# Kernel tuning notes

Measured on AMD Instinct MI355X. Metric: run time of the kernel, lower is better.

The kernel has to match this reference:

```python
import jax, jax.numpy as jnp
import numpy as np
import math

D_MODEL = 1024
N_HEADS = 16
HEAD_DIM = D_MODEL // N_HEADS


def _compute_slopes(n_heads: int) -> np.ndarray:
    def pow2_slopes(n):
        start = 2.0 ** (-(2.0 ** (-(math.log2(n) - 3))))
        return [start * (start ** i) for i in range(n)]
    if math.log2(n_heads).is_integer():
        s = pow2_slopes(n_heads)
    else:
        cp = 2 ** math.floor(math.log2(n_heads))
        s = pow2_slopes(cp) + pow2_slopes(2 * cp)[0::2][: n_heads - cp]
    return np.asarray(s, dtype=np.float32)


def setup_inputs() -> dict:
    key = jax.random.key(0)
    ks = jax.random.split(key, 11)
    B, T, D = 2, 2048, D_MODEL
    scale = 1.0 / math.sqrt(D)
    inp = {
        "query": jax.random.normal(ks[0], (B, T, D), jnp.float32),
        "key": jax.random.normal(ks[1], (B, T, D), jnp.float32),
        "value": jax.random.normal(ks[2], (B, T, D), jnp.float32),
        "Wq": jax.random.normal(ks[3], (D, D), jnp.float32) * scale,
        "bq": jnp.zeros((D,), jnp.float32),
        "Wk": jax.random.normal(ks[4], (D, D), jnp.float32) * scale,
        "bk": jnp.zeros((D,), jnp.float32),
        "Wv": jax.random.normal(ks[5], (D, D), jnp.float32) * scale,
        "bv": jnp.zeros((D,), jnp.float32),
        "Wo": jax.random.normal(ks[6], (D, D), jnp.float32) * scale,
        "bo": jnp.zeros((D,), jnp.float32),
    }
    return inp


def reference(query, key, value, Wq, bq, Wk, bk, Wv, bv, Wo, bo):
    B, Tq, D = query.shape
    Tk = key.shape[1]
    H, hd = N_HEADS, HEAD_DIM
    scale = hd ** -0.5

    # projections -> [B, H, T, hd]
    Q = (query @ Wq + bq).reshape(B, Tq, H, hd).transpose(0, 2, 1, 3)
    K = (key @ Wk + bk).reshape(B, Tk, H, hd).transpose(0, 2, 1, 3)
    V = (value @ Wv + bv).reshape(B, Tk, H, hd).transpose(0, 2, 1, 3)

    # scores [B, H, Tq, Tk]
    attn = jnp.einsum("bhqd,bhkd->bhqk", Q, K) * scale

    # ALiBi bias (only applied when Tq == Tk, mirroring the original)
    slopes = jnp.asarray(_compute_slopes(H))  # [H]
    pos = jnp.arange(Tq)
    dist = -jnp.abs(pos[None, :] - pos[:, None]).astype(jnp.float32)  # [Tq, Tk]
    bias = slopes[:, None, None] * dist[None]  # [H, Tq, Tk]
    attn = attn + bias[None]

    attn = jax.nn.softmax(attn, axis=-1)
    out = jnp.einsum("bhqk,bhkd->bhqd", attn, V)
    out = out.transpose(0, 2, 1, 3).reshape(B, Tq, D)
    return out @ Wo + bo
```

## Files before the change

### kernel.cpp

```cpp
#include <hip/hip_runtime.h>
#include <stdint.h>

#define BSZ 2
#define TT 2048
#define DD 1024
#define HH 16
#define HD 64

typedef __bf16 bf16x8 __attribute__((ext_vector_type(8)));
typedef float f32x4 __attribute__((ext_vector_type(4)));

#if __has_builtin(__builtin_amdgcn_exp2f)
#define EXP2(x) __builtin_amdgcn_exp2f(x)
#else
#define EXP2(x) exp2f(x)
#endif

__device__ __forceinline__ unsigned short f2bf(float f) {
    union { float f; unsigned u; } c; c.f = f;
    unsigned u = c.u;
    unsigned r = u + 0x7fffu + ((u >> 16) & 1u);
    return (unsigned short)(r >> 16);
}
__device__ __forceinline__ unsigned fasu(float f) {
    union { float f; unsigned u; } c; c.f = f; return c.u;
}

union U4BF { uint4 u; bf16x8 b; };
__device__ __forceinline__ bf16x8 as_bf8(uint4 v) { U4BF c; c.u = v; return c.b; }

#if __has_builtin(__builtin_amdgcn_global_load_lds)
__device__ __forceinline__ void gl_lds16(const ushort* g, ushort* l) {
    __builtin_amdgcn_global_load_lds(
        (const __attribute__((address_space(1))) uint32_t*)g,
        (__attribute__((address_space(3))) uint32_t*)l, 16, 0, 0);
}
#define GLL_LANE 1
#else
__device__ __forceinline__ void gl_lds16_fallback(const ushort* g, ushort* l, int lane) {
    *(uint4*)(l + lane * 8) = *(const uint4*)(g);
}
#define GLL_LANE 0
#endif

__global__ void cvt3(const float* __restrict__ q, const float* __restrict__ k,
                     const float* __restrict__ v, ushort* __restrict__ xq,
                     ushort* __restrict__ xk, ushort* __restrict__ xv, int n4) {
    int z = blockIdx.y;
    const float* in = (z == 0) ? q : (z == 1) ? k : v;
    ushort* out = (z == 0) ? xq : (z == 1) ? xk : xv;
    int i = blockIdx.x * blockDim.x + threadIdx.x;
    if (i < n4) {
        float4 val = ((const float4*)in)[i];
        ushort4 o;
        o.x = f2bf(val.x); o.y = f2bf(val.y); o.z = f2bf(val.z); o.w = f2bf(val.w);
        ((ushort4*)out)[i] = o;
    }
}

__global__ void wtrans(const float* __restrict__ W0, const float* __restrict__ W1,
                       const float* __restrict__ W2, const float* __restrict__ W3,
                       ushort* __restrict__ T0, ushort* __restrict__ T1,
                       ushort* __restrict__ T2, ushort* __restrict__ T3) {
    __shared__ float sh[32][33];
    const float* src; ushort* dst;
    switch (blockIdx.z) {
        case 0:  src = W0; dst = T0; break;
        case 1:  src = W1; dst = T1; break;
        case 2:  src = W2; dst = T2; break;
        default: src = W3; dst = T3; break;
    }
    int k0 = blockIdx.y * 32, n0 = blockIdx.x * 32;
    int tx = threadIdx.x, ty = threadIdx.y;
    sh[ty][tx] = src[(size_t)(k0 + ty) * DD + n0 + tx];
    __syncthreads();
    dst[(size_t)(n0 + ty) * DD + k0 + tx] = f2bf(sh[tx][ty]);
}

template<int BM, int OUT_MODE>
__global__ __launch_bounds__(256)
void gemm_mfma(const ushort* __restrict__ A0, const ushort* __restrict__ B0,
               const float* __restrict__ c0, void* __restrict__ d0,
               const ushort* __restrict__ A1, const ushort* __restrict__ B1,
               const float* __restrict__ c1, void* __restrict__ d1,
               const ushort* __restrict__ A2, const ushort* __restrict__ B2,
               const float* __restrict__ c2, void* __restrict__ d2) {
    constexpr int TI = 4;
    constexpr int TJ = (BM == 128) ? 4 : 2;
    constexpr int WC = (BM == 128) ? 2 : 4;
    __shared__ __attribute__((aligned(16))) ushort As[BM][32];
    __shared__ __attribute__((aligned(16))) ushort Bs[128][32];
    const ushort* A; const ushort* Bt; const float* bias; void* outp;
    const int z = blockIdx.z;
    switch (z) {
        case 0:  A = A0; Bt = B0; bias = c0; outp = d0; break;
        case 1:  A = A1; Bt = B1; bias = c1; outp = d1; break;
        default: A = A2; Bt = B2; bias = c2; outp = d2; break;
    }
    const int tid  = threadIdx.x;
    const int lane = tid & 63, w = tid >> 6;
    const int wr = w / WC, wc = w % WC;
    const int ln = lane & 15, quad = lane >> 4;
    const int m0 = blockIdx.y * BM, n0 = blockIdx.x * 128;

    const f32x4 zero = {0.f, 0.f, 0.f, 0.f};
    f32x4 acc[TI][TJ];
    #pragma unroll
    for (int i = 0; i < TI; ++i)
        #pragma unroll
        for (int j = 0; j < TJ; ++j) acc[i][j] = zero;

    const int lr  = lane >> 2;
    const int lc8 = (lane & 3) * 8;

    for (int kb = 0; kb < 1024; kb += 32) {
        #pragma unroll
        for (int it = 0; it < BM / 64; ++it) {
            int r0 = it * 64 + w * 16;
#if GLL_LANE
            gl_lds16(A + (size_t)(m0 + r0 + lr) * 1024 + kb + lc8, &As[r0][0]);
#else
            gl_lds16_fallback(A + (size_t)(m0 + r0 + lr) * 1024 + kb + lc8, &As[r0][0], lane);
#endif
        }
        #pragma unroll
        for (int it = 0; it < 2; ++it) {
            int r0 = it * 64 + w * 16;
#if GLL_LANE
            gl_lds16(Bt + (size_t)(n0 + r0 + lr) * 1024 + kb + lc8, &Bs[r0][0]);
#else
            gl_lds16_fallback(Bt + (size_t)(n0 + r0 + lr) * 1024 + kb + lc8, &Bs[r0][0], lane);
#endif
        }
        __syncthreads();
        bf16x8 af[TI], bfr[TJ];
        #pragma unroll
        for (int i = 0; i < TI; ++i)
            af[i] = as_bf8(*(const uint4*)&As[wr * 64 + i * 16 + ln][quad * 8]);
        #pragma unroll
        for (int j = 0; j < TJ; ++j)
            bfr[j] = as_bf8(*(const uint4*)&Bs[wc * (TJ * 16) + j * 16 + ln][quad * 8]);
        #pragma unroll
        for (int i = 0; i < TI; ++i)
            #pragma unroll
            for (int j = 0; j < TJ; ++j)
                acc[i][j] = __builtin_amdgcn_mfma_f32_16x16x32_bf16(af[i], bfr[j], acc[i][j], 0, 0, 0);
        __syncthreads();
    }

    #pragma unroll
    for (int j = 0; j < TJ; ++j) {
        int n = n0 + wc * (TJ * 16) + j * 16 + ln;
        float bv = bias[n];
        #pragma unroll
        for (int i = 0; i < TI; ++i) {
            int mb = m0 + wr * 64 + i * 16 + quad * 4;
            if (OUT_MODE == 0 && z == 2) {
                int b = mb >> 11, t = mb & 2047, h = n >> 6, d = n & 63;
                ushort4 pk;
                pk.x = f2bf(acc[i][j][0] + bv);
                pk.y = f2bf(acc[i][j][1] + bv);
                pk.z = f2bf(acc[i][j][2] + bv);
                pk.w = f2bf(acc[i][j][3] + bv);
                *(ushort4*)((ushort*)outp + ((size_t)((b * HH + h) * HD + d)) * TT + t) = pk;
            } else {
                #pragma unroll
                for (int r = 0; r < 4; ++r) {
                    int m = mb + r;
                    float v = acc[i][j][r] + bv;
                    if (OUT_MODE == 0) {
                        int b = m >> 11, t = m & 2047, h = n >> 6, d = n & 63;
                        ((ushort*)outp)[(((size_t)(b * HH + h)) * TT + t) * HD + d] = f2bf(v);
                    } else {
                        ((float*)outp)[(size_t)m * 1024 + n] = v;
                    }
                }
            }
        }
    }
}

__global__ __launch_bounds__(256)
void attn_kernel(const ushort* __restrict__ Qh, const ushort* __restrict__ Kh,
                 const ushort* __restrict__ Vtg, ushort* __restrict__ outp) {
    __shared__ __attribute__((aligned(16))) char smem[20992];
    ushort (*Ps)[32][72] = (ushort (*)[32][72])smem;
    float  (*Rbuf)[64][41] = (float (*)[64][41])smem;

    const int tid  = threadIdx.x;
    const int lane = tid & 63, w = tid >> 6;
    const int ln = lane & 15, quad = lane >> 4;

    bf16x8 ones;
    {
        union { ushort us[8]; bf16x8 v; } uu;
        #pragma unroll
        for (int p = 0; p < 8; ++p) uu.us[p] = 0x3F80;
        ones = uu.v;
    }
    const f32x4 zero = {0.f, 0.f, 0.f, 0.f};
    const float c1 = 0.125f * 1.44269504f;

    for (int sel = 0; sel < 2; ++sel) {
        __syncthreads();
        const int item = sel ? (2047 - (int)blockIdx.x) : (int)blockIdx.x;
        const int h = 15 - (item >> 7);
        const int rr = item & 127;
        const int b = rr & 1;
        const int qt = rr >> 1;
        const int bh = b * 16 + h;
        const int qbase = qt * 32;
        const float slope2 = exp2f(-0.5f * (float)(h + 1)) * 1.44269504f;
        const size_t base = (size_t)bh * (TT * HD);

        const int D = (int)ceilf(22.0f / slope2);
        int lo = qbase - D;
        int kt_lo = (lo > 0) ? (lo >> 6) : 0;
        int kt_hi = (qbase + 32 + D + 63) >> 6;
        if (kt_hi > TT / 64) kt_hi = TT / 64;
        const int nt = kt_hi - kt_lo;
        const int cs = (nt + 3) >> 2;
        const int my_lo = kt_lo + w * cs;
        const int my_hi = (my_lo + cs < kt_hi) ? (my_lo + cs) : kt_hi;

        bf16x8 qa[2][2];
        #pragma unroll
        for (int g = 0; g < 2; ++g) {
            const uint4* qp = (const uint4*)(Qh + base + (size_t)(qbase + g * 16 + ln) * HD);
            qa[g][0] = as_bf8(qp[quad]);
            qa[g][1] = as_bf8(qp[4 + quad]);
        }
        f32x4 o[2][4], lsum[2];
        #pragma unroll
        for (int g = 0; g < 2; ++g) {
            lsum[g] = zero;
            #pragma unroll
            for (int dn = 0; dn < 4; ++dn) o[g][dn] = zero;
        }
        float qrf[2][4];
        #pragma unroll
        for (int g = 0; g < 2; ++g)
            #pragma unroll
            for (int r = 0; r < 4; ++r)
                qrf[g][r] = (float)(qbase + g * 16 + quad * 4 + r);

        const ushort* kp = Kh  + base + (size_t)ln * HD + quad * 8;
        const ushort* vp = Vtg + base + (size_t)ln * TT + quad * 8;

        if (my_lo < my_hi) {
            uint4 kf[8];
            {
                const int ko = my_lo * 4096;
                #pragma unroll
                for (int n = 0; n < 4; ++n)
                    #pragma unroll
                    for (int hf = 0; hf < 2; ++hf)
                        kf[n * 2 + hf] = *(const uint4*)(kp + ko + n * 1024 + hf * 32);
            }

            for (int kt = my_lo; kt < my_hi; ++kt) {
                uint4 vf[8];
                {
                    const int vo = kt * 64;
                    #pragma unroll
                    for (int dn = 0; dn < 4; ++dn)
                        #pragma unroll
                        for (int hf = 0; hf < 2; ++hf)
                            vf[dn * 2 + hf] = *(const uint4*)(vp + dn * 32768 + vo + hf * 32);
                }
                uint4 kn[8];
                if (kt + 1 < my_hi) {
                    const int ko = (kt + 1) * 4096;
                    #pragma unroll
                    for (int n = 0; n < 4; ++n)
                        #pragma unroll
                        for (int hf = 0; hf < 2; ++hf)
                            kn[n * 2 + hf] = *(const uint4*)(kp + ko + n * 1024 + hf * 32);
                }

                f32x4 s[2][4];
                #pragma unroll
                for (int n = 0; n < 4; ++n) {
                    bf16x8 b0 = as_bf8(kf[n * 2]);
                    bf16x8 b1 = as_bf8(kf[n * 2 + 1]);
                    #pragma unroll
                    for (int g = 0; g < 2; ++g) {
                        f32x4 zz = zero;
                        zz = __builtin_amdgcn_mfma_f32_16x16x32_bf16(qa[g][0], b0, zz, 0, 0, 0);
                        s[g][n] = __builtin_amdgcn_mfma_f32_16x16x32_bf16(qa[g][1], b1, zz, 0, 0, 0);
                    }
                }

                #pragma unroll
                for (int n = 0; n < 4; ++n) {
                    float kg = (float)(kt * 64 + n * 16 + ln);
                    int bswz = ((2 * n + (ln >> 3)) ^ quad) * 8 + (ln & 7);
                    #pragma unroll
                    for (int g = 0; g < 2; ++g) {
                        #pragma unroll
                        for (int r = 0; r < 4; ++r) {
                            float d = qrf[g][r] - kg;
                            float arg = fmaf(s[g][n][r], c1, -slope2 * fabsf(d));
                            float p = EXP2(arg);
                            Ps[w][g * 16 + quad * 4 + r][bswz] = (ushort)(fasu(p) >> 16);
                        }
                    }
                }

                #pragma unroll
                for (int hf = 0; hf < 2; ++hf) {
                    bf16x8 ap0 = as_bf8(*(const uint4*)&Ps[w][ln]     [((hf * 4 + quad) ^ (ln >> 2)) * 8]);
                    bf16x8 ap1 = as_bf8(*(const uint4*)&Ps[w][16 + ln][((hf * 4 + quad) ^ (ln >> 2)) * 8]);
                    #pragma unroll
                    for (int dn = 0; dn < 4; ++dn) {
                        bf16x8 bv = as_bf8(vf[dn * 2 + hf]);
                        o[0][dn] = __builtin_amdgcn_mfma_f32_16x16x32_bf16(ap0, bv, o[0][dn], 0, 0, 0);
                        o[1][dn] = __builtin_amdgcn_mfma_f32_16x16x32_bf16(ap1, bv, o[1][dn], 0, 0, 0);
                    }
                    lsum[0] = __builtin_amdgcn_mfma_f32_16x16x32_bf16(ap0, ones, lsum[0], 0, 0, 0);
                    lsum[1] = __builtin_amdgcn_mfma_f32_16x16x32_bf16(ap1, ones, lsum[1], 0, 0, 0);
                }

                #pragma unroll
                for (int i = 0; i < 8; ++i) kf[i] = kn[i];
            }
        }

        __syncthreads();
        if (w >= 2) {
            float* dst = &Rbuf[w - 2][lane][0];
            #pragma unroll
            for (int g = 0; g < 2; ++g) {
                #pragma unroll
                for (int dn = 0; dn < 4; ++dn)
                    #pragma unroll
                    for (int r = 0; r < 4; ++r)
                        dst[g * 16 + dn * 4 + r] = o[g][dn][r];
                #pragma unroll
                for (int r = 0; r < 4; ++r)
                    dst[32 + g * 4 + r] = lsum[g][r];
            }
        }
        __syncthreads();
        if (w < 2) {
            const float* src = &Rbuf[w][lane][0];
            #pragma unroll
            for (int g = 0; g < 2; ++g) {
                #pragma unroll
                for (int dn = 0; dn < 4; ++dn)
                    #pragma unroll
                    for (int r = 0; r < 4; ++r)
                        o[g][dn][r] += src[g * 16 + dn * 4 + r];
                #pragma unroll
                for (int r = 0; r < 4; ++r)
                    lsum[g][r] += src[32 + g * 4 + r];
            }
        }
        __syncthreads();
        if (w == 1) {
            float* dst = &Rbuf[0][lane][0];
            #pragma unroll
            for (int g = 0; g < 2; ++g) {
                #pragma unroll
                for (int dn = 0; dn < 4; ++dn)
                    #pragma unroll
                    for (int r = 0; r < 4; ++r)
                        dst[g * 16 + dn * 4 + r] = o[g][dn][r];
                #pragma unroll
                for (int r = 0; r < 4; ++r)
                    dst[32 + g * 4 + r] = lsum[g][r];
            }
        }
        __syncthreads();
        if (w == 0) {
            const float* src = &Rbuf[0][lane][0];
            #pragma unroll
            for (int g = 0; g < 2; ++g) {
                #pragma unroll
                for (int dn = 0; dn < 4; ++dn)
                    #pragma unroll
                    for (int r = 0; r < 4; ++r)
                        o[g][dn][r] += src[g * 16 + dn * 4 + r];
                #pragma unroll
                for (int r = 0; r < 4; ++r)
                    lsum[g][r] += src[32 + g * 4 + r];
            }
            #pragma unroll
            for (int g = 0; g < 2; ++g) {
                #pragma unroll
                for (int r = 0; r < 4; ++r) {
                    float inv = __builtin_amdgcn_rcpf(lsum[g][r]);
                    int q = qbase + g * 16 + quad * 4 + r;
                    size_t ob = ((size_t)(b * TT + q)) * DD + h * HD;
                    #pragma unroll
                    for (int dn = 0; dn < 4; ++dn)
                        outp[ob + dn * 16 + ln] = f2bf(o[g][dn][r] * inv);
                }
            }
        }
    }
}

extern "C" void kernel_launch(void* const* d_in, const int* in_sizes, int n_in,
                              void* d_out, int out_size, void* d_ws, size_t ws_size,
                              hipStream_t stream) {
    const float* query = (const float*)d_in[0];
    const float* key   = (const float*)d_in[1];
    const float* value = (const float*)d_in[2];
    const float* Wq = (const float*)d_in[3];
    const float* bq = (const float*)d_in[4];
    const float* Wk = (const float*)d_in[5];
    const float* bk = (const float*)d_in[6];
    const float* Wv = (const float*)d_in[7];
    const float* bv = (const float*)d_in[8];
    const float* Wo = (const float*)d_in[9];
    const float* bo = (const float*)d_in[10];
    float* out = (float*)d_out;

    char* ws = (char*)d_ws;
    const size_t MB = 1024 * 1024;
    ushort* Xq  = (ushort*)(ws + 0);
    ushort* Xk  = (ushort*)(ws + 8 * MB);
    ushort* Xv  = (ushort*)(ws + 16 * MB);
    ushort* Wtq = (ushort*)(ws + 24 * MB);
    ushort* Wtk = (ushort*)(ws + 26 * MB);
    ushort* Wtv = (ushort*)(ws + 28 * MB);
    ushort* Wto = (ushort*)(ws + 30 * MB);
    ushort* Qh  = (ushort*)(ws + 32 * MB);
    ushort* Kh  = (ushort*)(ws + 40 * MB);
    ushort* Vt  = (ushort*)(ws + 48 * MB);
    ushort* attn = (ushort*)(ws + 0);

    const int n4 = (BSZ * TT * DD) / 4;
    cvt3<<<dim3(n4 / 256, 3), 256, 0, stream>>>(query, key, value, Xq, Xk, Xv, n4);
    wtrans<<<dim3(32, 32, 4), dim3(32, 32), 0, stream>>>(Wq, Wk, Wv, Wo, Wtq, Wtk, Wtv, Wto);

    gemm_mfma<128, 0><<<dim3(8, 32, 3), 256, 0, stream>>>(
        Xq, Wtq, bq, Qh,  Xk, Wtk, bk, Kh,  Xv, Wtv, bv, Vt);

    attn_kernel<<<dim3(1024), 256, 0, stream>>>(Qh, Kh, Vt, attn);

    gemm_mfma<64, 1><<<dim3(8, 64, 1), 256, 0, stream>>>(
        attn, Wto, bo, out,  attn, Wto, bo, out,  attn, Wto, bo, out);
}
```

Measured before the change: 248.5 us.

## Fuse prep kernels, add separate V transpose, tighten ALiBi window and reduction

Merges the fp32-to-bf16 input conversion and the weight transpose into one prep launch, with each transpose block now running 256 threads. The V projection no longer writes a transposed layout from its GEMM epilogue; a dedicated vtrans kernel transposes V through LDS instead. The attention kernel narrows the ALiBi band cutoff from 22 to 18 in log2 units, which skips more far-away keys but drops more probability mass. It also collapses the three-step cross-wave reduction into a single step with a larger LDS buffer and sets launch bounds for 4 blocks per CU, at the cost of one extra kernel launch and an extra pass over V.

```diff
diff --git a/kernel.cpp b/kernel.cpp
--- a/kernel.cpp
+++ b/kernel.cpp
@@ -11,9 +11,11 @@
 typedef float f32x4 __attribute__((ext_vector_type(4)));
 
 #if __has_builtin(__builtin_amdgcn_exp2f)
-#define EXP2(x) __builtin_amdgcn_exp2f(x)
+__device__ __forceinline__ float fexp2(float x) { return __builtin_amdgcn_exp2f(x); }
 #else
-#define EXP2(x) exp2f(x)
+__device__ __forceinline__ float fexp2(float x) {
+    float r; asm("v_exp_f32 %0, %1\n\ts_nop 1" : "=v"(r) : "v"(x)); return r;
+}
 #endif
 
 __device__ __forceinline__ unsigned short f2bf(float f) {
@@ -43,38 +45,69 @@
 #define GLL_LANE 0
 #endif
 
-__global__ void cvt3(const float* __restrict__ q, const float* __restrict__ k,
-                     const float* __restrict__ v, ushort* __restrict__ xq,
-                     ushort* __restrict__ xk, ushort* __restrict__ xv, int n4) {
-    int z = blockIdx.y;
-    const float* in = (z == 0) ? q : (z == 1) ? k : v;
-    ushort* out = (z == 0) ? xq : (z == 1) ? xk : xv;
-    int i = blockIdx.x * blockDim.x + threadIdx.x;
-    if (i < n4) {
+__global__ __launch_bounds__(256)
+void prep(const float* __restrict__ q, const float* __restrict__ k,
+          const float* __restrict__ v,
+          const float* __restrict__ W0, const float* __restrict__ W1,
+          const float* __restrict__ W2, const float* __restrict__ W3,
+          ushort* __restrict__ xq, ushort* __restrict__ xk, ushort* __restrict__ xv,
+          ushort* __restrict__ T0, ushort* __restrict__ T1,
+          ushort* __restrict__ T2, ushort* __restrict__ T3) {
+    __shared__ float sh[32][33];
+    const int y = blockIdx.y;
+    if (y < 3) {
+        const float* in = (y == 0) ? q : (y == 1) ? k : v;
+        ushort* out = (y == 0) ? xq : (y == 1) ? xk : xv;
+        int i = blockIdx.x * 256 + threadIdx.x;
         float4 val = ((const float4*)in)[i];
         ushort4 o;
         o.x = f2bf(val.x); o.y = f2bf(val.y); o.z = f2bf(val.z); o.w = f2bf(val.w);
         ((ushort4*)out)[i] = o;
-    }
-}
-
-__global__ void wtrans(const float* __restrict__ W0, const float* __restrict__ W1,
-                       const float* __restrict__ W2, const float* __restrict__ W3,
-                       ushort* __restrict__ T0, ushort* __restrict__ T1,
-                       ushort* __restrict__ T2, ushort* __restrict__ T3) {
-    __shared__ float sh[32][33];
-    const float* src; ushort* dst;
-    switch (blockIdx.z) {
-        case 0:  src = W0; dst = T0; break;
-        case 1:  src = W1; dst = T1; break;
-        case 2:  src = W2; dst = T2; break;
-        default: src = W3; dst = T3; break;
-    }
-    int k0 = blockIdx.y * 32, n0 = blockIdx.x * 32;
-    int tx = threadIdx.x, ty = threadIdx.y;
-    sh[ty][tx] = src[(size_t)(k0 + ty) * DD + n0 + tx];
+    } else {
+        const int x = blockIdx.x;
+        const float* src; ushort* dst;
+        switch (x >> 10) {
+            case 0:  src = W0; dst = T0; break;
+            case 1:  src = W1; dst = T1; break;
+            case 2:  src = W2; dst = T2; break;
+            default: src = W3; dst = T3; break;
+        }
+        const int tile = x & 1023;
+        const int k0 = (tile >> 5) * 32, n0 = (tile & 31) * 32;
+        const int tx = threadIdx.x & 31, ty = threadIdx.x >> 5;
+        #pragma unroll
+        for (int p = 0; p < 4; ++p)
+            sh[ty + 8 * p][tx] = src[(size_t)(k0 + ty + 8 * p) * DD + n0 + tx];
+        __syncthreads();
+        #pragma unroll
+        for (int p = 0; p < 4; ++p)
+            dst[(size_t)(n0 + ty + 8 * p) * DD + k0 + tx] = f2bf(sh[tx][ty + 8 * p]);
+    }
+}
+
+__global__ __launch_bounds__(256)
+void vtrans(const ushort* __restrict__ Vh, ushort* __restrict__ Vt) {
+    __shared__ ushort sh[64][72];
+    const int tid = threadIdx.x;
+    const int bh = blockIdx.y;
+    const int t0 = blockIdx.x * 64;
+    const size_t base = (size_t)bh * (TT * HD);
+    #pragma unroll
+    for (int it = 0; it < 2; ++it) {
+        int u = tid + it * 256;
+        int r = u >> 3, c8 = (u & 7) * 8;
+        *(uint4*)&sh[r][c8] = *(const uint4*)(Vh + base + (size_t)(t0 + r) * HD + c8);
+    }
     __syncthreads();
-    dst[(size_t)(n0 + ty) * DD + k0 + tx] = f2bf(sh[tx][ty]);
+    #pragma unroll
+    for (int it = 0; it < 2; ++it) {
+        int u = tid + it * 256;
+        int d = u >> 3, c8 = (u & 7) * 8;
+        alignas(16) ushort tmp[8];
+        #pragma unroll
+        for (int p = 0; p < 8; ++p) tmp[p] = sh[c8 + p][d];
+        *(uint4*)(Vt + base + (size_t)d * TT + t0 + c8) = *(const uint4*)tmp;
+    }
 }
 
 template<int BM, int OUT_MODE>
@@ -91,8 +124,7 @@
     __shared__ __attribute__((aligned(16))) ushort As[BM][32];
     __shared__ __attribute__((aligned(16))) ushort Bs[128][32];
     const ushort* A; const ushort* Bt; const float* bias; void* outp;
-    const int z = blockIdx.z;
-    switch (z) {
+    switch (blockIdx.z) {
         case 0:  A = A0; Bt = B0; bias = c0; outp = d0; break;
         case 1:  A = A1; Bt = B1; bias = c1; outp = d1; break;
         default: A = A2; Bt = B2; bias = c2; outp = d2; break;
@@ -154,38 +186,27 @@
         float bv = bias[n];
         #pragma unroll
         for (int i = 0; i < TI; ++i) {
-            int mb = m0 + wr * 64 + i * 16 + quad * 4;
-            if (OUT_MODE == 0 && z == 2) {
-                int b = mb >> 11, t = mb & 2047, h = n >> 6, d = n & 63;
-                ushort4 pk;
-                pk.x = f2bf(acc[i][j][0] + bv);
-                pk.y = f2bf(acc[i][j][1] + bv);
-                pk.z = f2bf(acc[i][j][2] + bv);
-                pk.w = f2bf(acc[i][j][3] + bv);
-                *(ushort4*)((ushort*)outp + ((size_t)((b * HH + h) * HD + d)) * TT + t) = pk;
-            } else {
-                #pragma unroll
-                for (int r = 0; r < 4; ++r) {
-                    int m = mb + r;
-                    float v = acc[i][j][r] + bv;
-                    if (OUT_MODE == 0) {
-                        int b = m >> 11, t = m & 2047, h = n >> 6, d = n & 63;
-                        ((ushort*)outp)[(((size_t)(b * HH + h)) * TT + t) * HD + d] = f2bf(v);
-                    } else {
-                        ((float*)outp)[(size_t)m * 1024 + n] = v;
-                    }
-                }
-            }
-        }
-    }
-}
-
-__global__ __launch_bounds__(256)
+            #pragma unroll
+            for (int r = 0; r < 4; ++r) {
+                int m = m0 + wr * 64 + i * 16 + quad * 4 + r;
+                float v = acc[i][j][r] + bv;
+                if (OUT_MODE == 0) {
+                    int b = m >> 11, t = m & 2047, h = n >> 6, d = n & 63;
+                    ((ushort*)outp)[(((size_t)(b * HH + h)) * TT + t) * HD + d] = f2bf(v);
+                } else {
+                    ((float*)outp)[(size_t)m * 1024 + n] = v;
+                }
+            }
+        }
+    }
+}
+
+__global__ __launch_bounds__(256, 4)
 void attn_kernel(const ushort* __restrict__ Qh, const ushort* __restrict__ Kh,
                  const ushort* __restrict__ Vtg, ushort* __restrict__ outp) {
-    __shared__ __attribute__((aligned(16))) char smem[20992];
+    __shared__ __attribute__((aligned(16))) char smem[33792];
     ushort (*Ps)[32][72] = (ushort (*)[32][72])smem;
-    float  (*Rbuf)[64][41] = (float (*)[64][41])smem;
+    float  (*Rbuf)[64][44] = (float (*)[64][44])smem;
 
     const int tid  = threadIdx.x;
     const int lane = tid & 63, w = tid >> 6;
@@ -213,7 +234,7 @@
         const float slope2 = exp2f(-0.5f * (float)(h + 1)) * 1.44269504f;
         const size_t base = (size_t)bh * (TT * HD);
 
-        const int D = (int)ceilf(22.0f / slope2);
+        const int D = (int)ceilf(18.0f / slope2);
         int lo = qbase - D;
         int kt_lo = (lo > 0) ? (lo >> 6) : 0;
         int kt_hi = (qbase + 32 + D + 63) >> 6;
@@ -301,7 +322,7 @@
                         for (int r = 0; r < 4; ++r) {
                             float d = qrf[g][r] - kg;
                             float arg = fmaf(s[g][n][r], c1, -slope2 * fabsf(d));
-                            float p = EXP2(arg);
+                            float p = fexp2(arg);
                             Ps[w][g * 16 + quad * 4 + r][bswz] = (ushort)(fasu(p) >> 16);
                         }
                     }
@@ -327,8 +348,8 @@
         }
 
         __syncthreads();
-        if (w >= 2) {
-            float* dst = &Rbuf[w - 2][lane][0];
+        if (w > 0) {
+            float* dst = &Rbuf[w - 1][lane][0];
             #pragma unroll
             for (int g = 0; g < 2; ++g) {
                 #pragma unroll
@@ -342,48 +363,21 @@
             }
         }
         __syncthreads();
-        if (w < 2) {
-            const float* src = &Rbuf[w][lane][0];
-            #pragma unroll
-            for (int g = 0; g < 2; ++g) {
-                #pragma unroll
-                for (int dn = 0; dn < 4; ++dn)
+        if (w == 0) {
+            #pragma unroll
+            for (int j = 0; j < 3; ++j) {
+                const float* src = &Rbuf[j][lane][0];
+                #pragma unroll
+                for (int g = 0; g < 2; ++g) {
+                    #pragma unroll
+                    for (int dn = 0; dn < 4; ++dn)
+                        #pragma unroll
+                        for (int r = 0; r < 4; ++r)
+                            o[g][dn][r] += src[g * 16 + dn * 4 + r];
                     #pragma unroll
                     for (int r = 0; r < 4; ++r)
-                        o[g][dn][r] += src[g * 16 + dn * 4 + r];
-                #pragma unroll
-                for (int r = 0; r < 4; ++r)
-                    lsum[g][r] += src[32 + g * 4 + r];
-            }
-        }
-        __syncthreads();
-        if (w == 1) {
-            float* dst = &Rbuf[0][lane][0];
-            #pragma unroll
-            for (int g = 0; g < 2; ++g) {
-                #pragma unroll
-                for (int dn = 0; dn < 4; ++dn)
-                    #pragma unroll
-                    for (int r = 0; r < 4; ++r)
-                        dst[g * 16 + dn * 4 + r] = o[g][dn][r];
-                #pragma unroll
-                for (int r = 0; r < 4; ++r)
-                    dst[32 + g * 4 + r] = lsum[g][r];
-            }
-        }
-        __syncthreads();
-        if (w == 0) {
-            const float* src = &Rbuf[0][lane][0];
-            #pragma unroll
-            for (int g = 0; g < 2; ++g) {
-                #pragma unroll
-                for (int dn = 0; dn < 4; ++dn)
-                    #pragma unroll
-                    for (int r = 0; r < 4; ++r)
-                        o[g][dn][r] += src[g * 16 + dn * 4 + r];
-                #pragma unroll
-                for (int r = 0; r < 4; ++r)
-                    lsum[g][r] += src[32 + g * 4 + r];
+                        lsum[g][r] += src[32 + g * 4 + r];
+                }
             }
             #pragma unroll
             for (int g = 0; g < 2; ++g) {
@@ -428,15 +422,17 @@
     ushort* Wto = (ushort*)(ws + 30 * MB);
     ushort* Qh  = (ushort*)(ws + 32 * MB);
     ushort* Kh  = (ushort*)(ws + 40 * MB);
-    ushort* Vt  = (ushort*)(ws + 48 * MB);
+    ushort* Vh  = (ushort*)(ws + 48 * MB);
+    ushort* Vt   = (ushort*)(ws + 16 * MB);
     ushort* attn = (ushort*)(ws + 0);
 
-    const int n4 = (BSZ * TT * DD) / 4;
-    cvt3<<<dim3(n4 / 256, 3), 256, 0, stream>>>(query, key, value, Xq, Xk, Xv, n4);
-    wtrans<<<dim3(32, 32, 4), dim3(32, 32), 0, stream>>>(Wq, Wk, Wv, Wo, Wtq, Wtk, Wtv, Wto);
+    prep<<<dim3(4096, 4), 256, 0, stream>>>(query, key, value, Wq, Wk, Wv, Wo,
+                                            Xq, Xk, Xv, Wtq, Wtk, Wtv, Wto);
 
     gemm_mfma<128, 0><<<dim3(8, 32, 3), 256, 0, stream>>>(
-        Xq, Wtq, bq, Qh,  Xk, Wtk, bk, Kh,  Xv, Wtv, bv, Vt);
+        Xq, Wtq, bq, Qh,  Xk, Wtk, bk, Kh,  Xv, Wtv, bv, Vh);
+
+    vtrans<<<dim3(TT / 64, BSZ * HH), 256, 0, stream>>>(Vh, Vt);
 
     attn_kernel<<<dim3(1024), 256, 0, stream>>>(Qh, Kh, Vt, attn);
 
```

Result: slower. 369.8 us (+48.8%).
